# Kernel tuning notes

Hardware: AMD Instinct MI355X
Metric: run time of the kernel (lower is better)

## Reference

```python
import jax, jax.numpy as jnp
import numpy as np

N_CLS = 4
NUM_QUERIES = 256
TEMPERATURE = 0.07
NEG_INF = -1e9


def setup_inputs() -> dict:
    key = jax.random.key(0)
    k1, k2, k3, k4, k5, k6 = jax.random.split(key, 6)
    B, C, H, W = 8, 512, 64, 64
    K = 3072
    pred_s = jax.random.normal(k1, (B, N_CLS, H, W), dtype=jnp.float32)
    feat_s_raw = jax.random.normal(k2, (B, C, H, W), dtype=jnp.float32)
    feat_t_raw = jax.random.normal(k3, (B, C, H, W), dtype=jnp.float32)
    target = jax.random.randint(k4, (B, H, W), 0, N_CLS, dtype=jnp.int64)
    queue = jax.random.normal(k5, (C, K), dtype=jnp.float32)
    queue = queue / jnp.linalg.norm(queue, axis=0, keepdims=True)  # F.normalize(queue, dim=0)
    queue_labels = jax.random.randint(k6, (1, K), 0, N_CLS, dtype=jnp.int64)
    return {"pred_s": pred_s, "feat_s_raw": feat_s_raw, "feat_t_raw": feat_t_raw,
            "target": target, "queue": queue, "queue_labels": queue_labels}


def _l2norm(x, axis):
    return x / jnp.clip(jnp.linalg.norm(x, axis=axis, keepdims=True), 1e-12)


def reference(pred_s, feat_s_raw, feat_t_raw, target, queue, queue_labels):
    # softmax over class dim (probs are only consumed in the hard (random=False)
    # branch of find_hard_sampling; module default is random=True)
    probs_s = jax.nn.softmax(pred_s, axis=1)
    fs = _l2norm(feat_s_raw, axis=1)   # [B, C, H, W]
    ft = _l2norm(feat_t_raw, axis=1)
    B, C, H, W = fs.shape

    # permute(0,2,3,1).flatten(0,2) -> [N, C], matching target.reshape(-1)
    rep = jnp.transpose(fs, (0, 2, 3, 1)).reshape(-1, C)
    rep_t = jnp.transpose(ft, (0, 2, 3, 1)).reshape(-1, C)
    tflat = target.reshape(-1)  # [N]

    # find_hard_sampling, random=True path: for each segment, draw NUM_QUERIES
    # indices uniformly from that segment's valid pixels (assumes every class
    # is present, which holds w.h.p. at this resolution).
    key = jax.random.key(42)
    keys = jax.random.split(key, N_CLS + 1)

    def sample_class(k, cls):
        logits = jnp.where(tflat == cls, 0.0, NEG_INF)  # uniform over valid pixels
        return jax.random.categorical(k, logits, shape=(NUM_QUERIES,))

    idx = jax.vmap(sample_class)(keys[:N_CLS], jnp.arange(N_CLS)).reshape(-1)  # [N_CLS*NQ]
    labels = jnp.repeat(jnp.arange(N_CLS), NUM_QUERIES)

    # shuffle (get_shuffle_ids)
    perm = jax.random.permutation(keys[N_CLS], idx.shape[0])
    idx = idx[perm]
    labels = labels[perm]

    feats_s = rep[idx]     # [n, C] random gather (memory-bound)
    feats_t = rep_t[idx]

    l_pos = jnp.einsum('nc,nc->n', feats_s, feats_t)[:, None]   # [n, 1]
    l_neg = jnp.einsum('nc,ck->nk', feats_s, queue)             # [n, K]
    logits = jnp.concatenate([l_pos, l_neg], axis=1) / TEMPERATURE

    # non-targeted mask: eq(labels_cur, queue_labels)
    mask = (labels[:, None] == queue_labels[0][None, :]).astype(logits.dtype)
    return logits, mask, labels
```

## Files before the change

### kernel.cpp

```cpp
#include <hip/hip_runtime.h>
#include <stdint.h>

#define N_PIX   32768
#define C_DIM   512
#define K_Q     3072
#define NCLS    4
#define NQ      256
#define N_SAMP  1024
#define HW      4096
#define L_ROW   3073

#define SCHEME 1

__host__ __device__ inline void tf2x32(uint32_t k0, uint32_t k1,
                                       uint32_t x0, uint32_t x1,
                                       uint32_t& o0, uint32_t& o1) {
  uint32_t ks2 = k0 ^ k1 ^ 0x1BD11BDAu;
  x0 += k0; x1 += k1;
#define ROTL_(v,d) (((v)<<(d))|((v)>>(32-(d))))
#define RND_(r) { x0 += x1; x1 = ROTL_(x1, r); x1 ^= x0; }
  RND_(13) RND_(15) RND_(26) RND_(6)
  x0 += k1; x1 += ks2 + 1u;
  RND_(17) RND_(29) RND_(16) RND_(24)
  x0 += ks2; x1 += k0 + 2u;
  RND_(13) RND_(15) RND_(26) RND_(6)
  x0 += k0; x1 += k1 + 3u;
  RND_(17) RND_(29) RND_(16) RND_(24)
  x0 += k1; x1 += ks2 + 4u;
  RND_(13) RND_(15) RND_(26) RND_(6)
  x0 += ks2; x1 += k0 + 5u;
  o0 = x0; o1 = x1;
#undef RND_
#undef ROTL_
}

__global__ void k_zero(int* cnt) {
  if (threadIdx.x < NCLS) cnt[threadIdx.x] = 0;
}

__global__ __launch_bounds__(256) void k_compact(const int* __restrict__ target,
                                                 int* __restrict__ cnt,
                                                 int* __restrict__ lists) {
  __shared__ int lcnt[NCLS];
  __shared__ int lbase[NCLS];
  int tid = threadIdx.x;
  if (tid < NCLS) lcnt[tid] = 0;
  __syncthreads();
  int p = blockIdx.x * 256 + tid;
  int c = target[p];
  int lpos = atomicAdd(&lcnt[c], 1);
  __syncthreads();
  if (tid < NCLS) lbase[tid] = atomicAdd(&cnt[tid], lcnt[tid]);
  __syncthreads();
  lists[c * N_PIX + lbase[c] + lpos] = p;
}

__global__ __launch_bounds__(256) void k_sample(
    const int* __restrict__ cnt, const int* __restrict__ lists,
    int* __restrict__ samp,
    uint32_t k0a, uint32_t k0b, uint32_t k1a, uint32_t k1b,
    uint32_t k2a, uint32_t k2b, uint32_t k3a, uint32_t k3b) {
  int c = blockIdx.y;
  int q = blockIdx.x;
  uint32_t ka, kb;
  if      (c == 0) { ka = k0a; kb = k0b; }
  else if (c == 1) { ka = k1a; kb = k1b; }
  else if (c == 2) { ka = k2a; kb = k2b; }
  else             { ka = k3a; kb = k3b; }

  int nv = cnt[c];
  const int* lst = lists + c * N_PIX;
  unsigned long long best = 0ull;
  for (int t = threadIdx.x; t < nv; t += 256) {
    int p = lst[t];
    uint32_t j = (uint32_t)(q * N_PIX + p);
    uint32_t o0, o1, bits;
    tf2x32(ka, kb, 0u, j, o0, o1);
    bits = o0 ^ o1;
    unsigned long long v =
        ((unsigned long long)(bits >> 9) << 15) | (unsigned)(32767 - p);
    if (v > best) best = v;
  }
  __shared__ unsigned long long red[256];
  red[threadIdx.x] = best;
  __syncthreads();
  for (int s = 128; s > 0; s >>= 1) {
    if (threadIdx.x < s && red[threadIdx.x + s] > red[threadIdx.x])
      red[threadIdx.x] = red[threadIdx.x + s];
    __syncthreads();
  }
  if (threadIdx.x == 0)
    samp[c * NQ + q] = 32767 - (int)(red[0] & 0x7FFFull);
}

__global__ __launch_bounds__(64) void k_perm(
    const int* __restrict__ samp, int* __restrict__ idx_final,
    int* __restrict__ labels_shuf, float* __restrict__ out_labels,
    uint32_t sk0, uint32_t sk1) {
  __shared__ uint32_t keys_s[N_SAMP];
  int lt = threadIdx.x;
  for (int t = lt; t < N_SAMP; t += 64) {
    uint32_t o0, o1;
    tf2x32(sk0, sk1, 0u, (uint32_t)t, o0, o1);
    keys_s[t] = o0 ^ o1;
  }
  __syncthreads();
  int i = blockIdx.x * 64 + lt;
  uint32_t ki = keys_s[i];
  int rank = 0;
#pragma unroll 4
  for (int j = 0; j < N_SAMP; ++j) {
    uint32_t kj = keys_s[j];
    rank += (int)((kj < ki) | ((kj == ki) & (j < i)));
  }
  idx_final[rank] = samp[i];
  int lab = i >> 8;
  labels_shuf[rank] = lab;
  out_labels[rank] = (float)lab;
}

__global__ __launch_bounds__(256) void k_gather(
    const float* __restrict__ fs, const float* __restrict__ ft,
    const int* __restrict__ idx_final, float* __restrict__ feats,
    float* __restrict__ out_logits) {
  int n = blockIdx.x;
  int p = idx_final[n];
  int b = p >> 12;
  int hw = p & (HW - 1);
  const float* fsb = fs + (size_t)b * C_DIM * HW + hw;
  const float* ftb = ft + (size_t)b * C_DIM * HW + hw;
  int c0 = threadIdx.x, c1 = threadIdx.x + 256;
  float s0 = fsb[(size_t)c0 * HW], s1 = fsb[(size_t)c1 * HW];
  float t0 = ftb[(size_t)c0 * HW], t1 = ftb[(size_t)c1 * HW];

  __shared__ float red[256];
  __shared__ float ns_sh, nt_sh;

  red[threadIdx.x] = s0 * s0 + s1 * s1;
  __syncthreads();
  for (int s = 128; s > 0; s >>= 1) {
    if (threadIdx.x < s) red[threadIdx.x] += red[threadIdx.x + s];
    __syncthreads();
  }
  if (threadIdx.x == 0) ns_sh = fmaxf(sqrtf(red[0]), 1e-12f);
  __syncthreads();

  red[threadIdx.x] = t0 * t0 + t1 * t1;
  __syncthreads();
  for (int s = 128; s > 0; s >>= 1) {
    if (threadIdx.x < s) red[threadIdx.x] += red[threadIdx.x + s];
    __syncthreads();
  }
  if (threadIdx.x == 0) nt_sh = fmaxf(sqrtf(red[0]), 1e-12f);
  __syncthreads();

  float ns = ns_sh, nt = nt_sh;
  float a0 = s0 / ns, a1 = s1 / ns;
  float b0 = t0 / nt, b1 = t1 / nt;
  feats[(size_t)n * C_DIM + c0] = a0;
  feats[(size_t)n * C_DIM + c1] = a1;

  red[threadIdx.x] = a0 * b0 + a1 * b1;
  __syncthreads();
  for (int s = 128; s > 0; s >>= 1) {
    if (threadIdx.x < s) red[threadIdx.x] += red[threadIdx.x + s];
    __syncthreads();
  }
  if (threadIdx.x == 0)
    out_logits[(size_t)n * L_ROW] = red[0] / 0.07f;
}

#define BM 64
#define BN 64
#define BK 32
__global__ __launch_bounds__(256) void k_gemm(
    const float* __restrict__ A,
    const float* __restrict__ Bq,
    const int* __restrict__ labels,
    const int* __restrict__ qlab,
    float* __restrict__ out) {
  __shared__ float As[BK][BM];
  __shared__ float Bs[BK][BN];
  int bm = blockIdx.x * BM;
  int bn = blockIdx.y * BN;
  int tid = threadIdx.x;
  int tx = tid & 15, ty = tid >> 4;

  float acc[4][4] = {};
  for (int k0 = 0; k0 < C_DIM; k0 += BK) {
#pragma unroll
    for (int it = 0; it < 2; ++it) {
      int lin = tid + it * 256;
      int r = lin >> 3;
      int g = lin & 7;
      float4 v = *(const float4*)(A + (size_t)(bm + r) * C_DIM + k0 + g * 4);
      As[g * 4 + 0][r] = v.x; As[g * 4 + 1][r] = v.y;
      As[g * 4 + 2][r] = v.z; As[g * 4 + 3][r] = v.w;
    }
#pragma unroll
    for (int it = 0; it < 2; ++it) {
      int lin = tid + it * 256;
      int kr = lin >> 4;
      int g = lin & 15;
      float4 v = *(const float4*)(Bq + (size_t)(k0 + kr) * K_Q + bn + g * 4);
      *(float4*)&Bs[kr][g * 4] = v;
    }
    __syncthreads();
#pragma unroll
    for (int k = 0; k < BK; ++k) {
      float a4[4], b4[4];
      *(float4*)a4 = *(const float4*)&As[k][ty * 4];
      *(float4*)b4 = *(const float4*)&Bs[k][tx * 4];
#pragma unroll
      for (int i = 0; i < 4; ++i)
#pragma unroll
        for (int j = 0; j < 4; ++j)
          acc[i][j] = fmaf(a4[i], b4[j], acc[i][j]);
    }
    __syncthreads();
  }

  float* out_mask = out + (size_t)N_SAMP * L_ROW;
#pragma unroll
  for (int i = 0; i < 4; ++i) {
    int row = bm + ty * 4 + i;
    int lab = labels[row];
    float* lrow = out + (size_t)row * L_ROW + 1 + bn + tx * 4;
    float* mrow = out_mask + (size_t)row * K_Q + bn + tx * 4;
#pragma unroll
    for (int j = 0; j < 4; ++j) {
      lrow[j] = acc[i][j] / 0.07f;
      mrow[j] = (lab == qlab[bn + tx * 4 + j]) ? 1.0f : 0.0f;
    }
  }
}

extern "C" void kernel_launch(void* const* d_in, const int* in_sizes, int n_in,
                              void* d_out, int out_size, void* d_ws, size_t ws_size,
                              hipStream_t stream) {
  const float* fs     = (const float*)d_in[1];
  const float* ft     = (const float*)d_in[2];
  const int*   target = (const int*)d_in[3];
  const float* queue  = (const float*)d_in[4];
  const int*   qlab   = (const int*)d_in[5];
  float* out = (float*)d_out;

  char* ws = (char*)d_ws;
  int*   cnt    = (int*)(ws + 0);
  int*   samp   = (int*)(ws + 256);
  int*   idxf   = (int*)(ws + 256 + 4096);
  int*   labs   = (int*)(ws + 256 + 8192);
  int*   lists  = (int*)(ws + 256 + 12288);
  float* feats  = (float*)(ws + 256 + 12288 + 4 * N_PIX * 4);

  uint32_t ck[5][2];
  for (int i = 0; i < 5; ++i)
    tf2x32(0u, 42u, 0u, (uint32_t)i, ck[i][0], ck[i][1]);
  uint32_t sk0, sk1;
  tf2x32(ck[4][0], ck[4][1], 0u, 1u, sk0, sk1);

  float* out_labels = out + (size_t)N_SAMP * L_ROW + (size_t)N_SAMP * K_Q;

  k_zero<<<1, 64, 0, stream>>>(cnt);
  k_compact<<<N_PIX / 256, 256, 0, stream>>>(target, cnt, lists);
  k_sample<<<dim3(NQ, NCLS), 256, 0, stream>>>(
      cnt, lists, samp,
      ck[0][0], ck[0][1], ck[1][0], ck[1][1],
      ck[2][0], ck[2][1], ck[3][0], ck[3][1]);
  k_perm<<<16, 64, 0, stream>>>(samp, idxf, labs, out_labels, sk0, sk1);
  k_gather<<<N_SAMP, 256, 0, stream>>>(fs, ft, idxf, feats, out);
  k_gemm<<<dim3(N_SAMP / BM, K_Q / BN), 256, 0, stream>>>(
      feats, queue, labs, qlab, out);
}
```

Measured before the change: 278.0 us.

## Use bf16x3 split MFMA GEMM with queue conversion and separate mask kernel

Both operands are split into bf16 hi/lo pairs: the queue by a new transpose-convert kernel, the features inside the gather kernel. The fp32 FMA GEMM is replaced by a 128x128-tile MFMA bf16 kernel that runs three partial products (hi*hi, lo*hi, hi*lo) over a 1536-long K, with swizzled LDS and register prefetch. The mask is written by its own kernel afterwards, and the mask region of the output is used as scratch for the bf16 operands until then. This moves the matmul onto matrix cores at a small accuracy cost from dropping the lo*lo term, and it adds a conversion pass plus an ordering dependency on the output scratch.

```diff
diff --git a/kernel.cpp b/kernel.cpp
--- a/kernel.cpp
+++ b/kernel.cpp
@@ -9,8 +9,19 @@
 #define N_SAMP  1024
 #define HW      4096
 #define L_ROW   3073
-
-#define SCHEME 1
+#define KH      1024
+#define KP      1536
+
+typedef float f32x4 __attribute__((ext_vector_type(4)));
+typedef short s16x8 __attribute__((ext_vector_type(8)));
+
+__device__ inline unsigned short f2bf(float f) {
+  uint32_t u = __float_as_uint(f);
+  return (unsigned short)((u + 0x7FFFu + ((u >> 16) & 1u)) >> 16);
+}
+__device__ inline float bf2f(unsigned short h) {
+  return __uint_as_float(((uint32_t)h) << 16);
+}
 
 __host__ __device__ inline void tf2x32(uint32_t k0, uint32_t k1,
                                        uint32_t x0, uint32_t x1,
@@ -74,9 +85,9 @@
   for (int t = threadIdx.x; t < nv; t += 256) {
     int p = lst[t];
     uint32_t j = (uint32_t)(q * N_PIX + p);
-    uint32_t o0, o1, bits;
+    uint32_t o0, o1;
     tf2x32(ka, kb, 0u, j, o0, o1);
-    bits = o0 ^ o1;
+    uint32_t bits = o0 ^ o1;
     unsigned long long v =
         ((unsigned long long)(bits >> 9) << 15) | (unsigned)(32767 - p);
     if (v > best) best = v;
@@ -121,7 +132,7 @@
 
 __global__ __launch_bounds__(256) void k_gather(
     const float* __restrict__ fs, const float* __restrict__ ft,
-    const int* __restrict__ idx_final, float* __restrict__ feats,
+    const int* __restrict__ idx_final, unsigned short* __restrict__ A2,
     float* __restrict__ out_logits) {
   int n = blockIdx.x;
   int p = idx_final[n];
@@ -157,8 +168,12 @@
   float ns = ns_sh, nt = nt_sh;
   float a0 = s0 / ns, a1 = s1 / ns;
   float b0 = t0 / nt, b1 = t1 / nt;
-  feats[(size_t)n * C_DIM + c0] = a0;
-  feats[(size_t)n * C_DIM + c1] = a1;
+
+  unsigned short h0 = f2bf(a0), h1 = f2bf(a1);
+  unsigned short l0 = f2bf(a0 - bf2f(h0)), l1 = f2bf(a1 - bf2f(h1));
+  unsigned short* row = A2 + (size_t)n * KH;
+  row[c0]       = h0;  row[c1]       = h1;
+  row[512 + c0] = l0;  row[512 + c1] = l1;
 
   red[threadIdx.x] = a0 * b0 + a1 * b1;
   __syncthreads();
@@ -167,71 +182,149 @@
     __syncthreads();
   }
   if (threadIdx.x == 0)
-    out_logits[(size_t)n * L_ROW] = red[0] / 0.07f;
-}
-
-#define BM 64
-#define BN 64
-#define BK 32
+    out_logits[(size_t)n * L_ROW] = red[0] * (1.0f / 0.07f);
+}
+
+__global__ __launch_bounds__(256) void k_convq(const float* __restrict__ queue,
+                                               unsigned short* __restrict__ B2) {
+  __shared__ float tile[64][65];
+  int tid = threadIdx.x;
+  int n0 = blockIdx.x * 64;
+  int k0 = blockIdx.y * 64;
+#pragma unroll
+  for (int it = 0; it < 4; ++it) {
+    int r = (tid >> 4) + it * 16;
+    int c4 = (tid & 15) * 4;
+    float4 v = *(const float4*)(queue + (size_t)(k0 + r) * K_Q + n0 + c4);
+    tile[r][c4 + 0] = v.x; tile[r][c4 + 1] = v.y;
+    tile[r][c4 + 2] = v.z; tile[r][c4 + 3] = v.w;
+  }
+  __syncthreads();
+  int tn = tid >> 2;
+  int kc = (tid & 3) * 16;
+  unsigned short* rowp = B2 + (size_t)(n0 + tn) * KH + k0 + kc;
+#pragma unroll
+  for (int g8 = 0; g8 < 2; ++g8) {
+    s16x8 vhi, vlo;
+#pragma unroll
+    for (int j = 0; j < 8; ++j) {
+      float v = tile[kc + g8 * 8 + j][tn];
+      unsigned short h = f2bf(v);
+      vhi[j] = (short)h;
+      vlo[j] = (short)f2bf(v - bf2f(h));
+    }
+    *(s16x8*)(rowp + g8 * 8)       = vhi;
+    *(s16x8*)(rowp + 512 + g8 * 8) = vlo;
+  }
+}
+
 __global__ __launch_bounds__(256) void k_gemm(
-    const float* __restrict__ A,
-    const float* __restrict__ Bq,
-    const int* __restrict__ labels,
-    const int* __restrict__ qlab,
+    const unsigned short* __restrict__ A2,
+    const unsigned short* __restrict__ B2,
     float* __restrict__ out) {
-  __shared__ float As[BK][BM];
-  __shared__ float Bs[BK][BN];
-  int bm = blockIdx.x * BM;
-  int bn = blockIdx.y * BN;
-  int tid = threadIdx.x;
-  int tx = tid & 15, ty = tid >> 4;
-
-  float acc[4][4] = {};
-  for (int k0 = 0; k0 < C_DIM; k0 += BK) {
-#pragma unroll
-    for (int it = 0; it < 2; ++it) {
-      int lin = tid + it * 256;
-      int r = lin >> 3;
-      int g = lin & 7;
-      float4 v = *(const float4*)(A + (size_t)(bm + r) * C_DIM + k0 + g * 4);
-      As[g * 4 + 0][r] = v.x; As[g * 4 + 1][r] = v.y;
-      As[g * 4 + 2][r] = v.z; As[g * 4 + 3][r] = v.w;
-    }
-#pragma unroll
-    for (int it = 0; it < 2; ++it) {
-      int lin = tid + it * 256;
-      int kr = lin >> 4;
-      int g = lin & 15;
-      float4 v = *(const float4*)(Bq + (size_t)(k0 + kr) * K_Q + bn + g * 4);
-      *(float4*)&Bs[kr][g * 4] = v;
-    }
-    __syncthreads();
-#pragma unroll
-    for (int k = 0; k < BK; ++k) {
-      float a4[4], b4[4];
-      *(float4*)a4 = *(const float4*)&As[k][ty * 4];
-      *(float4*)b4 = *(const float4*)&Bs[k][tx * 4];
-#pragma unroll
-      for (int i = 0; i < 4; ++i)
-#pragma unroll
-        for (int j = 0; j < 4; ++j)
-          acc[i][j] = fmaf(a4[i], b4[j], acc[i][j]);
-    }
-    __syncthreads();
-  }
-
-  float* out_mask = out + (size_t)N_SAMP * L_ROW;
-#pragma unroll
-  for (int i = 0; i < 4; ++i) {
-    int row = bm + ty * 4 + i;
-    int lab = labels[row];
-    float* lrow = out + (size_t)row * L_ROW + 1 + bn + tx * 4;
-    float* mrow = out_mask + (size_t)row * K_Q + bn + tx * 4;
-#pragma unroll
-    for (int j = 0; j < 4; ++j) {
-      lrow[j] = acc[i][j] / 0.07f;
-      mrow[j] = (lab == qlab[bn + tx * 4 + j]) ? 1.0f : 0.0f;
-    }
+  __shared__ unsigned short sAB[16384];
+  int tid  = threadIdx.x;
+  int lane = tid & 63;
+  int wave = tid >> 6;
+  int wm = wave >> 1, wn = wave & 1;
+  int bm = blockIdx.x * 128;
+  int bn = blockIdx.y * 128;
+
+  int rbase = wave * 32 + (lane >> 3);
+  int lcol  = (lane & 7) * 8;
+
+  f32x4 acc[4][4] = {};
+  s16x8 ra[4], rb[4];
+
+  const int NSTEP = KP / 64;
+  {
+#pragma unroll
+    for (int c = 0; c < 4; ++c) {
+      int r = rbase + c * 8;
+      ra[c] = *(const s16x8*)(A2 + (size_t)(bm + r) * KH + lcol);
+      rb[c] = *(const s16x8*)(B2 + (size_t)(bn + r) * KH + lcol);
+    }
+#pragma unroll
+    for (int c = 0; c < 4; ++c) {
+      int r = rbase + c * 8;
+      int slot = ((lane & 7) ^ (r & 7)) * 8;
+      *(s16x8*)&sAB[r * 64 + slot]        = ra[c];
+      *(s16x8*)&sAB[8192 + r * 64 + slot] = rb[c];
+    }
+  }
+  __syncthreads();
+
+  for (int s = 0; s < NSTEP; ++s) {
+    if (s + 1 < NSTEP) {
+      int kp = (s + 1) * 64;
+      int sA = (kp < 512) ? kp : kp - 512;
+      int sB = (kp < 1024) ? kp : kp - 1024;
+#pragma unroll
+      for (int c = 0; c < 4; ++c) {
+        int r = rbase + c * 8;
+        ra[c] = *(const s16x8*)(A2 + (size_t)(bm + r) * KH + sA + lcol);
+        rb[c] = *(const s16x8*)(B2 + (size_t)(bn + r) * KH + sB + lcol);
+      }
+    }
+#pragma unroll
+    for (int kk = 0; kk < 2; ++kk) {
+      int g = kk * 4 + (lane >> 4);
+      s16x8 af[4], bfr[4];
+#pragma unroll
+      for (int mi = 0; mi < 4; ++mi) {
+        int rowL = wm * 64 + mi * 16 + (lane & 15);
+        af[mi] = *(s16x8*)&sAB[rowL * 64 + ((g ^ (rowL & 7)) << 3)];
+      }
+#pragma unroll
+      for (int ni = 0; ni < 4; ++ni) {
+        int rowN = wn * 64 + ni * 16 + (lane & 15);
+        bfr[ni] = *(s16x8*)&sAB[8192 + rowN * 64 + ((g ^ (rowN & 7)) << 3)];
+      }
+#pragma unroll
+      for (int mi = 0; mi < 4; ++mi)
+#pragma unroll
+        for (int ni = 0; ni < 4; ++ni)
+          acc[mi][ni] = __builtin_amdgcn_mfma_f32_16x16x32_bf16(
+              af[mi], bfr[ni], acc[mi][ni], 0, 0, 0);
+    }
+    __syncthreads();
+    if (s + 1 < NSTEP) {
+#pragma unroll
+      for (int c = 0; c < 4; ++c) {
+        int r = rbase + c * 8;
+        int slot = ((lane & 7) ^ (r & 7)) * 8;
+        *(s16x8*)&sAB[r * 64 + slot]        = ra[c];
+        *(s16x8*)&sAB[8192 + r * 64 + slot] = rb[c];
+      }
+      __syncthreads();
+    }
+  }
+
+  const float sc = 1.0f / 0.07f;
+#pragma unroll
+  for (int mi = 0; mi < 4; ++mi) {
+#pragma unroll
+    for (int ni = 0; ni < 4; ++ni) {
+#pragma unroll
+      for (int j = 0; j < 4; ++j) {
+        int rl = wm * 64 + mi * 16 + ((lane >> 4) << 2) + j;
+        int cl = wn * 64 + ni * 16 + (lane & 15);
+        out[(size_t)(bm + rl) * L_ROW + 1 + (bn + cl)] = acc[mi][ni][j] * sc;
+      }
+    }
+  }
+}
+
+__global__ __launch_bounds__(256) void k_mask(const int* __restrict__ labels,
+                                              const int* __restrict__ qlab,
+                                              float* __restrict__ mask) {
+  int row = blockIdx.x;
+  int lab = labels[row];
+  float* mrow = mask + (size_t)row * K_Q;
+#pragma unroll
+  for (int j = 0; j < 12; ++j) {
+    int col = j * 256 + threadIdx.x;
+    mrow[col] = (lab == qlab[col]) ? 1.0f : 0.0f;
   }
 }
 
@@ -246,12 +339,15 @@
   float* out = (float*)d_out;
 
   char* ws = (char*)d_ws;
-  int*   cnt    = (int*)(ws + 0);
-  int*   samp   = (int*)(ws + 256);
-  int*   idxf   = (int*)(ws + 256 + 4096);
-  int*   labs   = (int*)(ws + 256 + 8192);
-  int*   lists  = (int*)(ws + 256 + 12288);
-  float* feats  = (float*)(ws + 256 + 12288 + 4 * N_PIX * 4);
+  int* cnt   = (int*)(ws + 0);
+  int* samp  = (int*)(ws + 4096);
+  int* idxf  = (int*)(ws + 8192);
+  int* labs  = (int*)(ws + 12288);
+  int* lists = (int*)(ws + 16384);
+
+  float* maskBase = out + (size_t)N_SAMP * L_ROW;
+  unsigned short* B2 = (unsigned short*)maskBase;
+  unsigned short* A2 = (unsigned short*)maskBase + (size_t)K_Q * KH;
 
   uint32_t ck[5][2];
   for (int i = 0; i < 5; ++i)
@@ -263,12 +359,13 @@
 
   k_zero<<<1, 64, 0, stream>>>(cnt);
   k_compact<<<N_PIX / 256, 256, 0, stream>>>(target, cnt, lists);
+  k_convq<<<dim3(K_Q / 64, C_DIM / 64), 256, 0, stream>>>(queue, B2);
   k_sample<<<dim3(NQ, NCLS), 256, 0, stream>>>(
       cnt, lists, samp,
       ck[0][0], ck[0][1], ck[1][0], ck[1][1],
       ck[2][0], ck[2][1], ck[3][0], ck[3][1]);
   k_perm<<<16, 64, 0, stream>>>(samp, idxf, labs, out_labels, sk0, sk1);
-  k_gather<<<N_SAMP, 256, 0, stream>>>(fs, ft, idxf, feats, out);
-  k_gemm<<<dim3(N_SAMP / BM, K_Q / BN), 256, 0, stream>>>(
-      feats, queue, labs, qlab, out);
-}
+  k_gather<<<N_SAMP, 256, 0, stream>>>(fs, ft, idxf, A2, out);
+  k_gemm<<<dim3(N_SAMP / 128, K_Q / 128), 256, 0, stream>>>(A2, B2, out);
+  k_mask<<<N_SAMP, 256, 0, stream>>>(labs, qlab, maskBase);
+}
```

After: 258.7 us. 1.07x faster.
